# Performance work log

Measured on AMD Instinct MI355X. Metric: run time of the kernel, lower is better.

Reference implementation:

```python
import jax, jax.numpy as jnp
import numpy as np

B, S, D, L, R = 8, 128, 512, 512, 50  # batch, seq_len, input_dim, linear_dim, n_rel_labels


def _head_params(key, n_out):
    k1, k2, k3, k4 = jax.random.split(key, 4)
    s1 = 1.0 / np.sqrt(2 * D)
    s2 = 1.0 / np.sqrt(L)
    return (jax.random.uniform(k1, (2 * D, L), jnp.float32, -s1, s1),
            jax.random.uniform(k2, (L,), jnp.float32, -s1, s1),
            jax.random.uniform(k3, (L, n_out), jnp.float32, -s2, s2),
            jax.random.uniform(k4, (n_out,), jnp.float32, -s2, s2))


def setup_inputs() -> dict:
    key = jax.random.key(0)
    kx, ks, kh, kt, kl = jax.random.split(key, 5)
    x = jax.random.normal(kx, (B, S, D), jnp.float32)
    span = _head_params(ks, 1)
    h2h = _head_params(kh, 1)
    t2t = _head_params(kt, 1)
    lab = _head_params(kl, R)
    return {
        'x': x,
        'span_W1': span[0], 'span_b1': span[1], 'span_W2': span[2], 'span_b2': span[3],
        'h2h_W1': h2h[0], 'h2h_b1': h2h[1], 'h2h_W2': h2h[2], 'h2h_b2': h2h[3],
        't2t_W1': t2t[0], 't2t_b1': t2t[1], 't2t_W2': t2t[2], 't2t_b2': t2t[3],
        'lab_W1': lab[0], 'lab_b1': lab[1], 'lab_W2': lab[2], 'lab_b2': lab[3],
    }


def _pair_head(x, W1, b1, W2, b2):
    # Linear on concat([x_i, x_j]) == x_i @ W_left + x_j @ W_right  (avoids [B,S,S,2D] concat)
    d = x.shape[-1]
    Wl, Wr = W1[:d], W1[d:]
    left = jnp.einsum('bid,dl->bil', x, Wl)   # [B,S,L]
    right = jnp.einsum('bjd,dl->bjl', x, Wr)  # [B,S,L]
    h = jnp.tanh(left[:, :, None, :] + right[:, None, :, :] + b1)  # [B,S,S,L]
    return jnp.einsum('bijl,lo->bijo', h, W2) + b2  # [B,S,S,n_out]


def reference(x, span_W1, span_b1, span_W2, span_b2,
              h2h_W1, h2h_b1, h2h_W2, h2h_b2,
              t2t_W1, t2t_b1, t2t_W2, t2t_b2,
              lab_W1, lab_b1, lab_W2, lab_b2):
    shst = _pair_head(x, span_W1, span_b1, span_W2, span_b2)[..., 0]  # [B,S,S]
    # torch: movedim(-1,1) -> triu + triu(1).T -> movedim(1,-1)
    bt = jnp.swapaxes(shst, 1, 2)
    sym = jnp.triu(bt) + jnp.swapaxes(jnp.triu(bt, 1), -1, -2)
    shst = jnp.swapaxes(sym, 1, 2)
    shoh = _pair_head(x, h2h_W1, h2h_b1, h2h_W2, h2h_b2)[..., 0]
    stot = _pair_head(x, t2t_W1, t2t_b1, t2t_W2, t2t_b2)[..., 0]
    shoh_labels = _pair_head(x, lab_W1, lab_b1, lab_W2, lab_b2)  # [B,S,S,R]
    return (shst, shoh, stot, shoh_labels)
```

## Files before the change

### kernel.cpp

```cpp
#include <hip/hip_runtime.h>

#define Bsz 8
#define Ssz 128
#define Dsz 512
#define D2 1024
#define Lsz 512
#define Rsz 50
#define SLOT 524288
#define BSLOT 65536
#define OUTMAT 131072

typedef __attribute__((ext_vector_type(8))) _Float16 f16x8;
typedef __attribute__((ext_vector_type(2))) __fp16 fp16x2;
typedef __attribute__((ext_vector_type(4))) float f32x4;

union UV4 { uint4 u; f16x8 h; };
union UH { unsigned short s; _Float16 h; };
union UP { fp16x2 h; unsigned u; };

struct K1Args {
  const float* W1[4];
  const float* b1[4];
};

__device__ __forceinline__ float f16lo(unsigned u) {
  UH x; x.s = (unsigned short)(u & 0xffffu); return (float)x.h;
}
__device__ __forceinline__ float f16hi(unsigned u) {
  UH x; x.s = (unsigned short)(u >> 16); return (float)x.h;
}
__device__ __forceinline__ float f16v(unsigned short s) {
  UH x; x.s = s; return (float)x.h;
}
__device__ __forceinline__ unsigned pkrtz(float a, float b) {
  UP c; c.h = __builtin_amdgcn_cvt_pkrtz(a, b); return c.u;
}
__device__ __forceinline__ unsigned short f2h(float v) {
  UH x; x.h = (_Float16)v; return x.s;
}
__device__ __forceinline__ float rcpf(float x) {
  return __builtin_amdgcn_rcpf(x);
}

__device__ __forceinline__ unsigned tanh2u(unsigned ea, unsigned eb) {
  UP a, b, p; a.u = ea; b.u = eb;
  const fp16x2 one = {(__fp16)1.0f, (__fp16)1.0f};
  p.h = a.h * b.h + one;
  const float h0 = fmaf(-2.0f, rcpf((float)p.h.x), 1.0f);
  const float h1 = fmaf(-2.0f, rcpf((float)p.h.y), 1.0f);
  return pkrtz(h0, h1);
}

__global__ __launch_bounds__(256) void prep_all(
    const float* __restrict__ x, K1Args a, const float* __restrict__ W2,
    const float* __restrict__ w2a, const float* __restrict__ w2b,
    const float* __restrict__ w2c,
    const float* __restrict__ b2a, const float* __restrict__ b2b,
    const float* __restrict__ b2c,
    unsigned short* __restrict__ W1F, unsigned short* __restrict__ X16F,
    unsigned short* __restrict__ W2F, float* __restrict__ Sums) {
  const int z = blockIdx.z;
  const int t = threadIdx.x;
  if (z < 4) {
    if (blockIdx.x >= 8) return;
    __shared__ float S[64][65];
    const float* __restrict__ W = a.W1[z];
    const int n0 = blockIdx.x * 64;
    const int k0 = blockIdx.y * 64;
    {
      const int kk = t >> 2, c16 = (t & 3) * 16;
      const float* p = W + (k0 + kk) * Lsz + n0 + c16;
#pragma unroll
      for (int c = 0; c < 4; ++c) {
        float4 v = *(const float4*)(p + c * 4);
        S[kk][c16 + c * 4 + 0] = v.x; S[kk][c16 + c * 4 + 1] = v.y;
        S[kk][c16 + c * 4 + 2] = v.z; S[kk][c16 + c * 4 + 3] = v.w;
      }
    }
    __syncthreads();
#pragma unroll
    for (int o = t; o < 512; o += 256) {
      const int lane = o & 63;
      const int ntl = (o >> 6) & 3, kbl = o >> 8;
      const int n_l = ntl * 16 + (lane & 15);
      const int k_l = kbl * 32 + (lane >> 4) * 8;
      uint4 pk;
      pk.x = pkrtz(S[k_l + 0][n_l], S[k_l + 1][n_l]);
      pk.y = pkrtz(S[k_l + 2][n_l], S[k_l + 3][n_l]);
      pk.z = pkrtz(S[k_l + 4][n_l], S[k_l + 5][n_l]);
      pk.w = pkrtz(S[k_l + 6][n_l], S[k_l + 7][n_l]);
      const long addr =
          ((long)((z * 32 + blockIdx.x * 4 + ntl) * 32 + blockIdx.y * 2 + kbl) *
               64 + lane) * 8;
      *(uint4*)(W1F + addr) = pk;
    }
  } else if (z == 4) {
    if (blockIdx.x >= 16) return;
    const int idx = (blockIdx.y * 16 + blockIdx.x) * 256 + t;
    const int frag = idx >> 6, lane = idx & 63;
    const int m = (frag >> 4) * 16 + (lane & 15);
    const int k0 = (frag & 15) * 32 + (lane >> 4) * 8;
    const float* p = x + m * Dsz + k0;
    float4 v0 = *(const float4*)p, v1 = *(const float4*)(p + 4);
    uint4 pk = make_uint4(pkrtz(v0.x, v0.y), pkrtz(v0.z, v0.w),
                          pkrtz(v1.x, v1.y), pkrtz(v1.z, v1.w));
    *(uint4*)(X16F + (long)idx * 8) = pk;
  } else {
    if (blockIdx.y != 0) return;
    if (blockIdx.x < 16) {
      const int idx = blockIdx.x * 256 + t;
      const int frag = idx >> 6, lane = idx & 63;
      const int o = (frag >> 4) * 16 + (lane & 15);
      const int k0 = (frag & 15) * 32 + (lane >> 4) * 8;
      float v[8];
#pragma unroll
      for (int e = 0; e < 8; ++e)
        v[e] = (o < Rsz) ? W2[(k0 + e) * Rsz + o] : 0.0f;
      uint4 pk = make_uint4(pkrtz(v[0], v[1]), pkrtz(v[2], v[3]),
                            pkrtz(v[4], v[5]), pkrtz(v[6], v[7]));
      *(uint4*)(W2F + (long)idx * 8) = pk;
    } else if (blockIdx.x < 19) {
      const int h = blockIdx.x - 16;
      const float* __restrict__ w2 = (h == 0) ? w2a : (h == 1 ? w2b : w2c);
      const float bb = (h == 0) ? b2a[0] : (h == 1 ? b2b[0] : b2c[0]);
      __shared__ float red[256];
      red[t] = w2[t] + w2[t + 256];
      __syncthreads();
      for (int s = 128; s > 0; s >>= 1) {
        if (t < s) red[t] += red[t + s];
        __syncthreads();
      }
      if (t == 0) Sums[h] = red[0] + bb;
    }
  }
}

__global__ __launch_bounds__(256) void gemm_lr_f16f(
    const unsigned short* __restrict__ X16F,
    const unsigned short* __restrict__ W1F, K1Args a,
    unsigned short* __restrict__ U) {
  const int side = blockIdx.z;
  const int h = side >> 1, r = side & 1;
  const float* __restrict__ bias = a.b1[h];
  const int tid = threadIdx.x;
  const int w = tid >> 6, lane = tid & 63;
  const int lm = lane & 15, q = lane >> 4;
  const int mtb = blockIdx.y * 4 + (w & 1) * 2;
  const int ntb = blockIdx.x * 4 + (w >> 1) * 2;

  f32x4 acc[2][2];
#pragma unroll
  for (int mt = 0; mt < 2; ++mt)
#pragma unroll
    for (int nt = 0; nt < 2; ++nt) {
      acc[mt][nt].x = 0.f; acc[mt][nt].y = 0.f;
      acc[mt][nt].z = 0.f; acc[mt][nt].w = 0.f;
    }

  for (int kb = 0; kb < 16; ++kb) {
    UV4 af[2], bf[2];
#pragma unroll
    for (int mt = 0; mt < 2; ++mt)
      af[mt].u = *(const uint4*)(X16F +
          ((long)((mtb + mt) * 16 + kb) * 64 + lane) * 8);
#pragma unroll
    for (int nt = 0; nt < 2; ++nt)
      bf[nt].u = *(const uint4*)(W1F +
          ((long)((h * 32 + ntb + nt) * 32 + r * 16 + kb) * 64 + lane) * 8);
#pragma unroll
    for (int mt = 0; mt < 2; ++mt)
#pragma unroll
      for (int nt = 0; nt < 2; ++nt)
        acc[mt][nt] = __builtin_amdgcn_mfma_f32_16x16x32_f16(
            af[mt].h, bf[nt].h, acc[mt][nt], 0, 0, 0);
  }

  unsigned short* slot = U + side * SLOT;
  if (h < 3) {
#pragma unroll
    for (int nt = 0; nt < 2; ++nt) {
      const int n_out = (ntb + nt) * 16 + lm;
      const float bb = (r == 0) ? bias[n_out] : 0.0f;
#pragma unroll
      for (int mt = 0; mt < 2; ++mt) {
        const int m0r = (mtb + mt) * 16 + q * 4;
        const float e0 = __expf(2.0f * (acc[mt][nt].x + bb));
        const float e1 = __expf(2.0f * (acc[mt][nt].y + bb));
        const float e2 = __expf(2.0f * (acc[mt][nt].z + bb));
        const float e3 = __expf(2.0f * (acc[mt][nt].w + bb));
        uint2 pr;
        pr.x = pkrtz(e0, e1);
        pr.y = pkrtz(e2, e3);
        const int bi = m0r >> 7, il = m0r & 127;
        *(uint2*)(slot + bi * BSLOT + n_out * Ssz + il) = pr;
      }
    }
  } else {
#pragma unroll
    for (int nt = 0; nt < 2; ++nt) {
      const int n_out = (ntb + nt) * 16 + lm;
      const float bb = (r == 0) ? bias[n_out] : 0.0f;
#pragma unroll
      for (int mt = 0; mt < 2; ++mt) {
#pragma unroll
        for (int reg = 0; reg < 4; ++reg) {
          const int m_out = (mtb + mt) * 16 + q * 4 + reg;
          float v;
          if (reg == 0) v = acc[mt][nt].x;
          else if (reg == 1) v = acc[mt][nt].y;
          else if (reg == 2) v = acc[mt][nt].z;
          else v = acc[mt][nt].w;
          slot[m_out * Lsz + n_out] = f2h(__expf(2.0f * (v + bb)));
        }
      }
    }
  }
}

__global__ __launch_bounds__(256) void pair_fused(
    const unsigned short* __restrict__ U,
    const unsigned short* __restrict__ W2F,
    const float* __restrict__ b2l,
    const float* __restrict__ w2a, const float* __restrict__ w2b,
    const float* __restrict__ w2c,
    float* __restrict__ P, float* __restrict__ out) {
  __shared__ unsigned short As[64][20];
  __shared__ unsigned short Bs[64][40];
  __shared__ float w2s[64];

  const int b = blockIdx.y;
  const int tid = threadIdx.x;

  if (blockIdx.x >= 192) {
    const int i = blockIdx.x - 192;
    const int w = tid >> 6, lane = tid & 63;
    const int lm = lane & 15, q = lane >> 4;
    const int jb = w * 32;

    const unsigned short* __restrict__ Lrow =
        U + 6 * SLOT + (b * Ssz + i) * Lsz;
    const unsigned short* __restrict__ Rb0 = U + 7 * SLOT + (long)b * Ssz * Lsz;
    float* out3 = out + 3 * OUTMAT;

    const unsigned short* Lb = Lrow + q * 8;
    const unsigned short* R0 = Rb0 + (jb + lm) * Lsz + q * 8;
    const unsigned short* R1 = Rb0 + (jb + 16 + lm) * Lsz + q * 8;
    const unsigned short* Bb = W2F + lane * 8;

    f32x4 acc[2][4];
#pragma unroll
    for (int mt = 0; mt < 2; ++mt)
#pragma unroll
      for (int nt = 0; nt < 4; ++nt) {
        acc[mt][nt].x = 0.f; acc[mt][nt].y = 0.f;
        acc[mt][nt].z = 0.f; acc[mt][nt].w = 0.f;
      }

#pragma unroll 2
    for (int c = 0; c < 8; ++c) {
      const uint4 lf0 = *(const uint4*)(Lb + c * 64);
      const uint4 lf1 = *(const uint4*)(Lb + c * 64 + 32);
#pragma unroll
      for (int kbl = 0; kbl < 2; ++kbl) {
        const uint4 lf = kbl ? lf1 : lf0;
        UV4 bfr[4];
#pragma unroll
        for (int nt = 0; nt < 4; ++nt)
          bfr[nt].u =
              *(const uint4*)(Bb + (long)(nt * 16 + kbl + 2 * c) * 512);
#pragma unroll
        for (int mt = 0; mt < 2; ++mt) {
          const uint4 rv =
              *(const uint4*)((mt ? R1 : R0) + c * 64 + kbl * 32);
          UV4 A;
          A.u = make_uint4(tanh2u(lf.x, rv.x), tanh2u(lf.y, rv.y),
                           tanh2u(lf.z, rv.z), tanh2u(lf.w, rv.w));
#pragma unroll
          for (int nt = 0; nt < 4; ++nt)
            acc[mt][nt] = __builtin_amdgcn_mfma_f32_16x16x32_f16(
                A.h, bfr[nt].h, acc[mt][nt], 0, 0, 0);
        }
      }
    }

#pragma unroll
    for (int nt = 0; nt < 4; ++nt) {
      const int o = nt * 16 + lm;
      if (o >= Rsz) continue;
      const float bias = b2l[o];
#pragma unroll
      for (int mt = 0; mt < 2; ++mt) {
#pragma unroll
        for (int reg = 0; reg < 4; ++reg) {
          const int j = jb + mt * 16 + q * 4 + reg;
          const long base = ((long)((b * Ssz + i) * Ssz) + j) * Rsz;
          float v;
          if (reg == 0) v = acc[mt][nt].x;
          else if (reg == 1) v = acc[mt][nt].y;
          else if (reg == 2) v = acc[mt][nt].z;
          else v = acc[mt][nt].w;
          out3[base + o] = v + bias;
        }
      }
    }
  } else {
    const int tile = blockIdx.x >> 1;
    const int lhalf = blockIdx.x & 1;
    const int h = tile >> 5;
    const int r = tile & 31;
    const int it = r >> 2, jt = r & 3;
    const int i0 = it * 16, j0 = jt * 32;
    if (h == 0 && i0 + 15 < j0) return;
    const int t = tid;
    const int tj = t & 31;
    const int th = t >> 5;
    const int lb = lhalf * 256;
    const int tjE = tj & ~1;
    const int bsh = (tj & 1) * 16;

    const unsigned short* __restrict__ A  = U + (2 * h) * SLOT + b * BSLOT;
    const unsigned short* __restrict__ Bt = U + (2 * h + 1) * SLOT + b * BSLOT;
    const float* __restrict__ w2 = (h == 0) ? w2a : (h == 1 ? w2b : w2c);

    float acc0 = 0.f, acc1 = 0.f;
    const int sr = t >> 2;
    const int scA = (t & 3) * 4;
    const int scB = (t & 3) * 8;

    for (int lc = lb; lc < lb + 256; lc += 64) {
      __syncthreads();
      *(uint2*)&As[sr][scA] = *(const uint2*)(A + (lc + sr) * Ssz + i0 + scA);
      *(uint4*)&Bs[sr][scB] = *(const uint4*)(Bt + (lc + sr) * Ssz + j0 + scB);
      if (t < 64) w2s[t] = w2[lc + t];
      __syncthreads();
#pragma unroll 4
      for (int l = 0; l < 64; l += 2) {
        const unsigned ua0 = *(const unsigned*)&As[l][th * 2];
        const unsigned ua1 = *(const unsigned*)&As[l + 1][th * 2];
        const unsigned ub0 = *(const unsigned*)&Bs[l][tjE];
        const unsigned ub1 = *(const unsigned*)&Bs[l + 1][tjE];
        const float2 wv = *(const float2*)&w2s[l];
        const float b0 = f16v((unsigned short)(ub0 >> bsh));
        const float b1 = f16v((unsigned short)(ub1 >> bsh));
        acc0 = fmaf(wv.x, rcpf(fmaf(f16lo(ua0), b0, 1.0f)), acc0);
        acc1 = fmaf(wv.x, rcpf(fmaf(f16hi(ua0), b0, 1.0f)), acc1);
        acc0 = fmaf(wv.y, rcpf(fmaf(f16lo(ua1), b1, 1.0f)), acc0);
        acc1 = fmaf(wv.y, rcpf(fmaf(f16hi(ua1), b1, 1.0f)), acc1);
      }
    }

    const int i = i0 + th * 2, j = j0 + tj;
    float* Ph = P + ((long)(lhalf * 3 + h) * Bsz + b) * 16384;
    Ph[i * Ssz + j] = acc0;
    Ph[(i + 1) * Ssz + j] = acc1;
  }
}

__global__ __launch_bounds__(256) void combine_sc(
    const float* __restrict__ P, const float* __restrict__ Sums,
    float* __restrict__ out) {
  const int ck = blockIdx.x, b = blockIdx.y, h = blockIdx.z;
  const int t = threadIdx.x;
  const float Sh = Sums[h];
  const float* P0 = P + ((long)(0 * 3 + h) * Bsz + b) * 16384;
  const float* P1 = P + ((long)(1 * 3 + h) * Bsz + b) * 16384;
  if (h == 0) {
#pragma unroll
    for (int k = 0; k < 8; ++k) {
      const int idx = ck * 2048 + k * 256 + t;
      const int i = idx >> 7, j = idx & 127;
      if (j > i) continue;
      const float v = fmaf(-2.0f, P0[idx] + P1[idx], Sh);
      out[(b * Ssz + i) * Ssz + j] = v;
      out[(b * Ssz + j) * Ssz + i] = v;
    }
  } else {
    float* o = out + h * OUTMAT + b * 16384;
#pragma unroll
    for (int k = 0; k < 8; ++k) {
      const int idx = ck * 2048 + k * 256 + t;
      o[idx] = fmaf(-2.0f, P0[idx] + P1[idx], Sh);
    }
  }
}

extern "C" void kernel_launch(void* const* d_in, const int* in_sizes, int n_in,
                              void* d_out, int out_size, void* d_ws,
                              size_t ws_size, hipStream_t stream) {
  (void)in_sizes; (void)n_in; (void)out_size; (void)ws_size;
  const float* x = (const float*)d_in[0];
  K1Args a;
  a.W1[0] = (const float*)d_in[1];  a.b1[0] = (const float*)d_in[2];
  a.W1[1] = (const float*)d_in[5];  a.b1[1] = (const float*)d_in[6];
  a.W1[2] = (const float*)d_in[9];  a.b1[2] = (const float*)d_in[10];
  a.W1[3] = (const float*)d_in[13]; a.b1[3] = (const float*)d_in[14];
  const float* w2a = (const float*)d_in[3];
  const float* b2a = (const float*)d_in[4];
  const float* w2b = (const float*)d_in[7];
  const float* b2b = (const float*)d_in[8];
  const float* w2c = (const float*)d_in[11];
  const float* b2c = (const float*)d_in[12];
  const float* W2l = (const float*)d_in[15];
  const float* b2l = (const float*)d_in[16];
  float* out = (float*)d_out;

  unsigned short* U    = (unsigned short*)d_ws;
  unsigned short* W1F  = U + 8 * SLOT;
  unsigned short* X16F = U + 8 * SLOT + 4 * (Lsz * D2);
  unsigned short* W2F  = U + 8 * SLOT + 5 * (Lsz * D2);
  float* Sums = (float*)(W2F + 64 * Lsz);
  float* P = Sums + 4;

  prep_all<<<dim3(19, 16, 6), 256, 0, stream>>>(
      x, a, W2l, w2a, w2b, w2c, b2a, b2b, b2c, W1F, X16F, W2F, Sums);
  gemm_lr_f16f<<<dim3(8, 16, 8), 256, 0, stream>>>(X16F, W1F, a, U);
  pair_fused<<<dim3(320, Bsz), 256, 0, stream>>>(
      U, W2F, b2l, w2a, w2b, w2c, P, out);
  combine_sc<<<dim3(8, Bsz, 3), 256, 0, stream>>>(P, Sums, out);
}
```

Before: 167.9 us.

## Fuse combine kernel into pair kernel and double per-block work

The scalar heads no longer split the L reduction into two halves written to a partial buffer. Each block now reduces over all of L and applies the final -2*acc+Sum transform and the symmetric write directly, which removes the combine_sc launch and the partial-buffer round trip. The label-head blocks now process two rows i each in a sequential loop, halving the grid from 320 to 160 blocks per batch. The cost is less parallelism and longer per-block serial work, which may leave CUs underused.

```diff
diff --git a/kernel.cpp b/kernel.cpp
--- a/kernel.cpp
+++ b/kernel.cpp
@@ -222,8 +222,8 @@
     const unsigned short* __restrict__ W2F,
     const float* __restrict__ b2l,
     const float* __restrict__ w2a, const float* __restrict__ w2b,
-    const float* __restrict__ w2c,
-    float* __restrict__ P, float* __restrict__ out) {
+    const float* __restrict__ w2c, const float* __restrict__ Sums,
+    float* __restrict__ out) {
   __shared__ unsigned short As[64][20];
   __shared__ unsigned short Bs[64][40];
   __shared__ float w2s[64];
@@ -231,81 +231,84 @@
   const int b = blockIdx.y;
   const int tid = threadIdx.x;
 
-  if (blockIdx.x >= 192) {
-    const int i = blockIdx.x - 192;
+  if (blockIdx.x >= 96) {
+    const int ib = (blockIdx.x - 96) * 2;
     const int w = tid >> 6, lane = tid & 63;
     const int lm = lane & 15, q = lane >> 4;
     const int jb = w * 32;
 
-    const unsigned short* __restrict__ Lrow =
-        U + 6 * SLOT + (b * Ssz + i) * Lsz;
     const unsigned short* __restrict__ Rb0 = U + 7 * SLOT + (long)b * Ssz * Lsz;
     float* out3 = out + 3 * OUTMAT;
 
-    const unsigned short* Lb = Lrow + q * 8;
     const unsigned short* R0 = Rb0 + (jb + lm) * Lsz + q * 8;
     const unsigned short* R1 = Rb0 + (jb + 16 + lm) * Lsz + q * 8;
     const unsigned short* Bb = W2F + lane * 8;
 
-    f32x4 acc[2][4];
-#pragma unroll
-    for (int mt = 0; mt < 2; ++mt)
+#pragma unroll 1
+    for (int pass = 0; pass < 2; ++pass) {
+      const int i = ib + pass;
+      const unsigned short* Lb =
+          U + 6 * SLOT + (b * Ssz + i) * Lsz + q * 8;
+
+      f32x4 acc[2][4];
+#pragma unroll
+      for (int mt = 0; mt < 2; ++mt)
+#pragma unroll
+        for (int nt = 0; nt < 4; ++nt) {
+          acc[mt][nt].x = 0.f; acc[mt][nt].y = 0.f;
+          acc[mt][nt].z = 0.f; acc[mt][nt].w = 0.f;
+        }
+
+#pragma unroll 2
+      for (int c = 0; c < 8; ++c) {
+        const uint4 lf0 = *(const uint4*)(Lb + c * 64);
+        const uint4 lf1 = *(const uint4*)(Lb + c * 64 + 32);
+#pragma unroll
+        for (int kbl = 0; kbl < 2; ++kbl) {
+          const uint4 lf = kbl ? lf1 : lf0;
+          UV4 bfr[4];
+#pragma unroll
+          for (int nt = 0; nt < 4; ++nt)
+            bfr[nt].u =
+                *(const uint4*)(Bb + (long)(nt * 16 + kbl + 2 * c) * 512);
+#pragma unroll
+          for (int mt = 0; mt < 2; ++mt) {
+            const uint4 rv =
+                *(const uint4*)((mt ? R1 : R0) + c * 64 + kbl * 32);
+            UV4 A;
+            A.u = make_uint4(tanh2u(lf.x, rv.x), tanh2u(lf.y, rv.y),
+                             tanh2u(lf.z, rv.z), tanh2u(lf.w, rv.w));
+#pragma unroll
+            for (int nt = 0; nt < 4; ++nt)
+              acc[mt][nt] = __builtin_amdgcn_mfma_f32_16x16x32_f16(
+                  A.h, bfr[nt].h, acc[mt][nt], 0, 0, 0);
+          }
+        }
+      }
+
 #pragma unroll
       for (int nt = 0; nt < 4; ++nt) {
-        acc[mt][nt].x = 0.f; acc[mt][nt].y = 0.f;
-        acc[mt][nt].z = 0.f; acc[mt][nt].w = 0.f;
-      }
-
-#pragma unroll 2
-    for (int c = 0; c < 8; ++c) {
-      const uint4 lf0 = *(const uint4*)(Lb + c * 64);
-      const uint4 lf1 = *(const uint4*)(Lb + c * 64 + 32);
-#pragma unroll
-      for (int kbl = 0; kbl < 2; ++kbl) {
-        const uint4 lf = kbl ? lf1 : lf0;
-        UV4 bfr[4];
-#pragma unroll
-        for (int nt = 0; nt < 4; ++nt)
-          bfr[nt].u =
-              *(const uint4*)(Bb + (long)(nt * 16 + kbl + 2 * c) * 512);
+        const int o = nt * 16 + lm;
+        if (o >= Rsz) continue;
+        const float bias = b2l[o];
 #pragma unroll
         for (int mt = 0; mt < 2; ++mt) {
-          const uint4 rv =
-              *(const uint4*)((mt ? R1 : R0) + c * 64 + kbl * 32);
-          UV4 A;
-          A.u = make_uint4(tanh2u(lf.x, rv.x), tanh2u(lf.y, rv.y),
-                           tanh2u(lf.z, rv.z), tanh2u(lf.w, rv.w));
-#pragma unroll
-          for (int nt = 0; nt < 4; ++nt)
-            acc[mt][nt] = __builtin_amdgcn_mfma_f32_16x16x32_f16(
-                A.h, bfr[nt].h, acc[mt][nt], 0, 0, 0);
+#pragma unroll
+          for (int reg = 0; reg < 4; ++reg) {
+            const int j = jb + mt * 16 + q * 4 + reg;
+            const long base = ((long)((b * Ssz + i) * Ssz) + j) * Rsz;
+            float v;
+            if (reg == 0) v = acc[mt][nt].x;
+            else if (reg == 1) v = acc[mt][nt].y;
+            else if (reg == 2) v = acc[mt][nt].z;
+            else v = acc[mt][nt].w;
+            out3[base + o] = v + bias;
+          }
         }
       }
     }
-
-#pragma unroll
-    for (int nt = 0; nt < 4; ++nt) {
-      const int o = nt * 16 + lm;
-      if (o >= Rsz) continue;
-      const float bias = b2l[o];
-#pragma unroll
-      for (int mt = 0; mt < 2; ++mt) {
-#pragma unroll
-        for (int reg = 0; reg < 4; ++reg) {
-          const int j = jb + mt * 16 + q * 4 + reg;
-          const long base = ((long)((b * Ssz + i) * Ssz) + j) * Rsz;
-          float v;
-          if (reg == 0) v = acc[mt][nt].x;
-          else if (reg == 1) v = acc[mt][nt].y;
-          else if (reg == 2) v = acc[mt][nt].z;
-          else v = acc[mt][nt].w;
-          out3[base + o] = v + bias;
-        }
-      }
-    }
   } else {
-    const int tile = blockIdx.x >> 1;
-    const int lhalf = blockIdx.x & 1;
+    const int tile = blockIdx.x;
     const int h = tile >> 5;
     const int r = tile & 31;
     const int it = r >> 2, jt = r & 3;
@@ -314,7 +317,6 @@
     const int t = tid;
     const int tj = t & 31;
     const int th = t >> 5;
-    const int lb = lhalf * 256;
     const int tjE = tj & ~1;
     const int bsh = (tj & 1) * 16;
 
@@ -327,7 +329,7 @@
     const int scA = (t & 3) * 4;
     const int scB = (t & 3) * 8;
 
-    for (int lc = lb; lc < lb + 256; lc += 64) {
+    for (int lc = 0; lc < Lsz; lc += 64) {
       __syncthreads();
       *(uint2*)&As[sr][scA] = *(const uint2*)(A + (lc + sr) * Ssz + i0 + scA);
       *(uint4*)&Bs[sr][scB] = *(const uint4*)(Bt + (lc + sr) * Ssz + j0 + scB);
@@ -349,37 +351,23 @@
       }
     }
 
+    const float Sh = Sums[h];
+    const float v0 = fmaf(-2.0f, acc0, Sh);
+    const float v1 = fmaf(-2.0f, acc1, Sh);
     const int i = i0 + th * 2, j = j0 + tj;
-    float* Ph = P + ((long)(lhalf * 3 + h) * Bsz + b) * 16384;
-    Ph[i * Ssz + j] = acc0;
-    Ph[(i + 1) * Ssz + j] = acc1;
-  }
-}
-
-__global__ __launch_bounds__(256) void combine_sc(
-    const float* __restrict__ P, const float* __restrict__ Sums,
-    float* __restrict__ out) {
-  const int ck = blockIdx.x, b = blockIdx.y, h = blockIdx.z;
-  const int t = threadIdx.x;
-  const float Sh = Sums[h];
-  const float* P0 = P + ((long)(0 * 3 + h) * Bsz + b) * 16384;
-  const float* P1 = P + ((long)(1 * 3 + h) * Bsz + b) * 16384;
-  if (h == 0) {
-#pragma unroll
-    for (int k = 0; k < 8; ++k) {
-      const int idx = ck * 2048 + k * 256 + t;
-      const int i = idx >> 7, j = idx & 127;
-      if (j > i) continue;
-      const float v = fmaf(-2.0f, P0[idx] + P1[idx], Sh);
-      out[(b * Ssz + i) * Ssz + j] = v;
-      out[(b * Ssz + j) * Ssz + i] = v;
-    }
-  } else {
-    float* o = out + h * OUTMAT + b * 16384;
-#pragma unroll
-    for (int k = 0; k < 8; ++k) {
-      const int idx = ck * 2048 + k * 256 + t;
-      o[idx] = fmaf(-2.0f, P0[idx] + P1[idx], Sh);
+    if (h == 0) {
+      if (j <= i) {
+        out[(b * Ssz + i) * Ssz + j] = v0;
+        out[(b * Ssz + j) * Ssz + i] = v0;
+      }
+      if (j <= i + 1) {
+        out[(b * Ssz + i + 1) * Ssz + j] = v1;
+        out[(b * Ssz + j) * Ssz + (i + 1)] = v1;
+      }
+    } else {
+      float* o = out + h * OUTMAT;
+      o[(b * Ssz + i) * Ssz + j] = v0;
+      o[(b * Ssz + i + 1) * Ssz + j] = v1;
     }
   }
 }
@@ -409,12 +397,10 @@
   unsigned short* X16F = U + 8 * SLOT + 4 * (Lsz * D2);
   unsigned short* W2F  = U + 8 * SLOT + 5 * (Lsz * D2);
   float* Sums = (float*)(W2F + 64 * Lsz);
-  float* P = Sums + 4;
 
   prep_all<<<dim3(19, 16, 6), 256, 0, stream>>>(
       x, a, W2l, w2a, w2b, w2c, b2a, b2b, b2c, W1F, X16F, W2F, Sums);
   gemm_lr_f16f<<<dim3(8, 16, 8), 256, 0, stream>>>(X16F, W1F, a, U);
-  pair_fused<<<dim3(320, Bsz), 256, 0, stream>>>(
-      U, W2F, b2l, w2a, w2b, w2c, P, out);
-  combine_sc<<<dim3(8, Bsz, 3), 256, 0, stream>>>(P, Sums, out);
-}
+  pair_fused<<<dim3(160, Bsz), 256, 0, stream>>>(
+      U, W2F, b2l, w2a, w2b, w2c, Sums, out);
+}
```

Measured after the change: 169.2 us. No clear change (+0.8%).
